# Performance work log

Measured on AMD Instinct MI355X. Metric: run time of the kernel, lower is better.

The kernel has to match this reference:

```python
import jax, jax.numpy as jnp
import numpy as np

CLASS_W, COORD_W = 2.0, 5.0
ALPHA, GAMMA = 0.25, 2.0
NUM_SAMPLE_POINTS = 100
MATCH_NUM = 13
INF = 1e8


def _bernstein_matrix(n):
    t = jnp.linspace(0.0, 1.0, n, dtype=jnp.float32)
    return jnp.stack([(1 - t) ** 3, 3 * t * (1 - t) ** 2,
                      3 * t ** 2 * (1 - t), t ** 3], axis=1)  # [n, 4]


def _sample_bezier(ctrl):  # ctrl: [N, 4, 2] -> [N, n*2]
    B = _bernstein_matrix(NUM_SAMPLE_POINTS)
    pts = jnp.einsum('sk,nkd->nsd', B, ctrl)
    return pts.reshape(ctrl.shape[0], -1)


def setup_inputs() -> dict:
    key = jax.random.key(0)
    k1, k2, k3, k4 = jax.random.split(key, 4)
    bs, nq, nc, n_gt = 4, 1000, 1, 32
    return {
        'pred_logits': jax.random.normal(k1, (bs, nq, nc), dtype=jnp.float32),
        'pred_beziers': jax.random.uniform(k2, (bs, nq, 8), dtype=jnp.float32),
        'tgt_labels': jax.random.randint(k3, (bs, n_gt), 0, nc).astype(jnp.int64),
        'tgt_beziers': jax.random.uniform(k4, (bs, n_gt, 4, 2), dtype=jnp.float32),
    }


def _cost_matrix(pred_logits, pred_beziers, tgt_labels, tgt_beziers):
    bs, nq, nc = pred_logits.shape
    n_gt = tgt_labels.shape[1]
    out_prob = jax.nn.sigmoid(pred_logits.reshape(bs * nq, nc))
    tgt_ids = tgt_labels.reshape(-1)
    neg = (1 - ALPHA) * out_prob ** GAMMA * (-jnp.log1p(-out_prob + 1e-8))
    pos = ALPHA * (1 - out_prob) ** GAMMA * (-jnp.log(out_prob + 1e-8))
    cost_class = pos[:, tgt_ids] - neg[:, tgt_ids]        # [bs*nq, bs*n_gt]
    out_pts = _sample_bezier(pred_beziers.reshape(-1, 4, 2))   # [bs*nq, S*2]
    tgt_pts = _sample_bezier(tgt_beziers.reshape(-1, 4, 2))    # [bs*n_gt, S*2]
    cost_coord = jnp.sum(jnp.abs(out_pts[:, None, :] - tgt_pts[None, :, :]), axis=-1)
    C = CLASS_W * cost_class + COORD_W * cost_coord       # [bs*nq, bs*n_gt]
    C4 = C.reshape(bs, nq, bs, n_gt)
    # per-image block (equivalent of C.split(sizes, -1) with c[i])
    return C4[jnp.arange(bs), :, jnp.arange(bs), :]       # [bs, nq, n_gt]


def _assign(c):  # c: [nq, n_gt]
    nq, n_gt = c.shape
    # k smallest queries per target (torch.topk largest=False along dim 0)
    _, idx = jax.lax.top_k(-c.T, MATCH_NUM)               # [n_gt, k]
    src = idx.reshape(-1)                                  # [n_gt*k]
    cols = jnp.repeat(jnp.arange(n_gt), MATCH_NUM)
    cost_inf = jnp.full((nq, n_gt), INF, dtype=c.dtype)
    cost_inf = cost_inf.at[src, cols].set(c[src, cols])
    min_idx = jnp.argmin(cost_inf, axis=1)                 # [nq]
    # sorted unique of src, padded with sentinel nq (jit-friendly torch.unique)
    s = jnp.sort(src)
    keep = jnp.concatenate([jnp.array([True]), s[1:] != s[:-1]])
    uniq = jnp.sort(jnp.where(keep, s, nq))
    count = keep.sum().astype(jnp.int32)
    tgt = jnp.where(uniq < nq, min_idx[jnp.clip(uniq, 0, nq - 1)], -1)
    return uniq, tgt, count


def reference(pred_logits, pred_beziers, tgt_labels, tgt_beziers):
    c = _cost_matrix(pred_logits, pred_beziers, tgt_labels, tgt_beziers)
    src_u, tgt_u, counts = jax.vmap(_assign)(c)
    # src_u/tgt_u: [bs, n_gt*MATCH_NUM], valid entries = first counts[i], rest padded
    return src_u, tgt_u, counts
```

## Files before the change

kernel.cpp:

```cpp
#include <hip/hip_runtime.h>
#include <stdint.h>

#define NQ 1000
#define NGT 32
#define BS 4
#define NSP 100
#define MNUM 13
#define NPAIR (NGT * MNUM)
#define QPB 8

__device__ __forceinline__ unsigned int f2sort(float f) {
    unsigned int u = __float_as_uint(f);
    return (u & 0x80000000u) ? ~u : (u | 0x80000000u);
}

__global__ __launch_bounds__(256) void cost_kernel(
    const float* __restrict__ logits,
    const float* __restrict__ pbez,
    const float* __restrict__ tbez,
    float* __restrict__ C)
{
    const int blk = blockIdx.x;
    const int b  = blk / (NQ / QPB);
    const int qc = blk % (NQ / QPB);
    const int tid = threadIdx.x;

    __shared__ float tpts[NGT][201];
    __shared__ float ppts[QPB][201];
    __shared__ float cls[QPB];

    for (int idx = tid; idx < NGT * NSP; idx += 256) {
        const int g = idx / NSP, s = idx % NSP;
        const float t   = (float)s * (1.0f / 99.0f);
        const float omt = 1.0f - t;
        const float b0 = omt * omt * omt;
        const float b1 = 3.0f * t * omt * omt;
        const float b2 = 3.0f * t * t * omt;
        const float b3 = t * t * t;
        const float* c8 = tbez + ((size_t)b * NGT + g) * 8;
        tpts[g][2 * s]     = b0 * c8[0] + b1 * c8[2] + b2 * c8[4] + b3 * c8[6];
        tpts[g][2 * s + 1] = b0 * c8[1] + b1 * c8[3] + b2 * c8[5] + b3 * c8[7];
    }
    for (int idx = tid; idx < QPB * NSP; idx += 256) {
        const int ql = idx / NSP, s = idx % NSP;
        const int q = qc * QPB + ql;
        const float t   = (float)s * (1.0f / 99.0f);
        const float omt = 1.0f - t;
        const float b0 = omt * omt * omt;
        const float b1 = 3.0f * t * omt * omt;
        const float b2 = 3.0f * t * t * omt;
        const float b3 = t * t * t;
        const float* c8 = pbez + ((size_t)b * NQ + q) * 8;
        ppts[ql][2 * s]     = b0 * c8[0] + b1 * c8[2] + b2 * c8[4] + b3 * c8[6];
        ppts[ql][2 * s + 1] = b0 * c8[1] + b1 * c8[3] + b2 * c8[5] + b3 * c8[7];
    }
    if (tid < QPB) {
        const int q = qc * QPB + tid;
        const float lg = logits[(size_t)b * NQ + q];
        float p;
        if (lg >= 0.0f) { p = 1.0f / (1.0f + expf(-lg)); }
        else            { const float e = expf(lg); p = e / (1.0f + e); }
        const float pos = 0.25f * (1.0f - p) * (1.0f - p) * (-logf(p + 1e-8f));
        const float neg = 0.75f * p * p * (-log1pf(-p + 1e-8f));
        cls[tid] = pos - neg;
    }
    __syncthreads();

    const int ql = tid >> 5;
    const int g  = tid & 31;
    double acc = 0.0;
    #pragma unroll 8
    for (int i = 0; i < 2 * NSP; ++i)
        acc += (double)fabsf(ppts[ql][i] - tpts[g][i]);
    const int q = qc * QPB + ql;
    C[((size_t)b * NQ + q) * NGT + g] = 2.0f * cls[ql] + 5.0f * (float)acc;
}

__global__ __launch_bounds__(64) void select_kernel(
    const float* __restrict__ C,
    int* __restrict__ sel)
{
    const int blk = blockIdx.x;
    const int b = blk / NGT, g = blk % NGT;
    const int lane = threadIdx.x;

    unsigned long long loc[16];
    #pragma unroll
    for (int j = 0; j < 16; ++j) {
        const int q = j * 64 + lane;
        if (q < NQ) {
            const float c = C[((size_t)b * NQ + q) * NGT + g];
            loc[j] = ((unsigned long long)f2sort(c) << 32) | (unsigned int)q;
        } else {
            loc[j] = ~0ull;
        }
    }
    for (int r = 0; r < MNUM; ++r) {
        unsigned long long m = loc[0];
        #pragma unroll
        for (int j = 1; j < 16; ++j) m = (loc[j] < m) ? loc[j] : m;
        #pragma unroll
        for (int off = 1; off < 64; off <<= 1) {
            const unsigned long long o = __shfl_xor(m, off, 64);
            m = (o < m) ? o : m;
        }
        const int q = (int)(m & 0xFFFFFFFFu);
        if (lane == (q & 63)) loc[q >> 6] = ~0ull;
        if (lane == 0) sel[blk * MNUM + r] = q;
    }
}

__global__ __launch_bounds__(256) void assemble_kernel(
    const float* __restrict__ C,
    const int* __restrict__ sel,
    int* __restrict__ out)
{
    const int b = blockIdx.x;
    const int tid = threadIdx.x;

    __shared__ unsigned long long key[NQ];
    __shared__ int cnts[256];
    __shared__ int offs[257];

    for (int q = tid; q < NQ; q += 256) key[q] = ~0ull;
    __syncthreads();

    for (int j = tid; j < NPAIR; j += 256) {
        const int g = j / MNUM;
        const int q = sel[(b * NGT + g) * MNUM + (j % MNUM)];
        const float c = C[((size_t)b * NQ + q) * NGT + g];
        const unsigned long long k =
            ((unsigned long long)f2sort(c) << 32) | (unsigned int)g;
        atomicMin(&key[q], k);
    }
    __syncthreads();

    const int base = tid * 4;
    int lc = 0;
    for (int k = 0; k < 4; ++k) {
        const int q = base + k;
        if (q < NQ && key[q] != ~0ull) lc++;
    }
    cnts[tid] = lc;
    __syncthreads();
    if (tid == 0) {
        int run = 0;
        for (int i = 0; i < 256; ++i) { offs[i] = run; run += cnts[i]; }
        offs[256] = run;
    }
    __syncthreads();

    const int total = offs[256];
    int* src_out = out + b * NPAIR;
    int* tgt_out = out + BS * NPAIR + b * NPAIR;

    int pos = offs[tid];
    for (int k = 0; k < 4; ++k) {
        const int q = base + k;
        if (q < NQ && key[q] != ~0ull) {
            src_out[pos] = q;
            tgt_out[pos] = (int)(key[q] & 0xFFFFFFFFu);
            pos++;
        }
    }
    for (int i = total + tid; i < NPAIR; i += 256) {
        src_out[i] = NQ;
        tgt_out[i] = -1;
    }
    if (tid == 0) out[2 * BS * NPAIR + b] = total;
}

extern "C" void kernel_launch(void* const* d_in, const int* in_sizes, int n_in,
                              void* d_out, int out_size, void* d_ws, size_t ws_size,
                              hipStream_t stream) {
    const float* logits = (const float*)d_in[0];
    const float* pbez   = (const float*)d_in[1];
    const float* tbez   = (const float*)d_in[3];

    float* C   = (float*)d_ws;
    int*   sel = (int*)((char*)d_ws + (size_t)BS * NQ * NGT * sizeof(float));
    int*   out = (int*)d_out;

    cost_kernel<<<BS * (NQ / QPB), 256, 0, stream>>>(logits, pbez, tbez, C);
    select_kernel<<<BS * NGT, 64, 0, stream>>>(C, sel);
    assemble_kernel<<<BS, 256, 0, stream>>>(C, sel, out);
}
```

Baseline: 86.33 us.

## Fuse cost, top-k select and assemble into one kernel with per-image flag sync

Replaces the three-kernel pipeline with one kernel in which each block owns one (image, target) column. The block computes that column of the cost matrix in shared memory, recomputing each query's Bezier samples on the fly, then runs the 13-smallest selection locally. The selected indices and sort keys go to a workspace, and one block per image spins on MAGIC flags before doing the unique/argmin assembly. This removes two launches and the global cost-matrix round trip. In exchange, each prediction curve is sampled 32 times instead of once. Correctness relies on all blocks being co-resident for the spin-wait, and the flags are never reset, so a later call can see stale MAGIC values.

```diff
diff --git a/kernel.cpp b/kernel.cpp
--- a/kernel.cpp
+++ b/kernel.cpp
@@ -7,131 +7,139 @@
 #define NSP 100
 #define MNUM 13
 #define NPAIR (NGT * MNUM)
-#define QPB 8
+#define MAGIC 0x5A5A5A5Au
+
+#define SEL_WORDS 32
+#define FLAG_BASE (128 * SEL_WORDS)
 
 __device__ __forceinline__ unsigned int f2sort(float f) {
     unsigned int u = __float_as_uint(f);
     return (u & 0x80000000u) ? ~u : (u | 0x80000000u);
 }
 
-__global__ __launch_bounds__(256) void cost_kernel(
+__global__ __launch_bounds__(256) void fused_matcher_kernel(
     const float* __restrict__ logits,
     const float* __restrict__ pbez,
     const float* __restrict__ tbez,
-    float* __restrict__ C)
+    unsigned int* __restrict__ ws,
+    int* __restrict__ out)
 {
     const int blk = blockIdx.x;
-    const int b  = blk / (NQ / QPB);
-    const int qc = blk % (NQ / QPB);
+    const int b = blk >> 5;
+    const int g = blk & 31;
     const int tid = threadIdx.x;
 
-    __shared__ float tpts[NGT][201];
-    __shared__ float ppts[QPB][201];
-    __shared__ float cls[QPB];
+    __shared__ float bas[NSP][4];
+    __shared__ float tp[2 * NSP];
+    __shared__ float colC[NQ];
+    __shared__ int          selq_s[MNUM];
+    __shared__ unsigned int selk_s[MNUM];
+    __shared__ unsigned long long key[NQ];
+    __shared__ int cnts[256];
+    __shared__ int offs[257];
 
-    for (int idx = tid; idx < NGT * NSP; idx += 256) {
-        const int g = idx / NSP, s = idx % NSP;
-        const float t   = (float)s * (1.0f / 99.0f);
+    if (tid < NSP) {
+        const float t   = (float)tid * (1.0f / 99.0f);
         const float omt = 1.0f - t;
         const float b0 = omt * omt * omt;
         const float b1 = 3.0f * t * omt * omt;
         const float b2 = 3.0f * t * t * omt;
         const float b3 = t * t * t;
+        bas[tid][0] = b0; bas[tid][1] = b1; bas[tid][2] = b2; bas[tid][3] = b3;
         const float* c8 = tbez + ((size_t)b * NGT + g) * 8;
-        tpts[g][2 * s]     = b0 * c8[0] + b1 * c8[2] + b2 * c8[4] + b3 * c8[6];
-        tpts[g][2 * s + 1] = b0 * c8[1] + b1 * c8[3] + b2 * c8[5] + b3 * c8[7];
-    }
-    for (int idx = tid; idx < QPB * NSP; idx += 256) {
-        const int ql = idx / NSP, s = idx % NSP;
-        const int q = qc * QPB + ql;
-        const float t   = (float)s * (1.0f / 99.0f);
-        const float omt = 1.0f - t;
-        const float b0 = omt * omt * omt;
-        const float b1 = 3.0f * t * omt * omt;
-        const float b2 = 3.0f * t * t * omt;
-        const float b3 = t * t * t;
-        const float* c8 = pbez + ((size_t)b * NQ + q) * 8;
-        ppts[ql][2 * s]     = b0 * c8[0] + b1 * c8[2] + b2 * c8[4] + b3 * c8[6];
-        ppts[ql][2 * s + 1] = b0 * c8[1] + b1 * c8[3] + b2 * c8[5] + b3 * c8[7];
-    }
-    if (tid < QPB) {
-        const int q = qc * QPB + tid;
-        const float lg = logits[(size_t)b * NQ + q];
-        float p;
-        if (lg >= 0.0f) { p = 1.0f / (1.0f + expf(-lg)); }
-        else            { const float e = expf(lg); p = e / (1.0f + e); }
-        const float pos = 0.25f * (1.0f - p) * (1.0f - p) * (-logf(p + 1e-8f));
-        const float neg = 0.75f * p * p * (-log1pf(-p + 1e-8f));
-        cls[tid] = pos - neg;
+        tp[2 * tid]     = b0 * c8[0] + b1 * c8[2] + b2 * c8[4] + b3 * c8[6];
+        tp[2 * tid + 1] = b0 * c8[1] + b1 * c8[3] + b2 * c8[5] + b3 * c8[7];
     }
     __syncthreads();
 
-    const int ql = tid >> 5;
-    const int g  = tid & 31;
-    double acc = 0.0;
-    #pragma unroll 8
-    for (int i = 0; i < 2 * NSP; ++i)
-        acc += (double)fabsf(ppts[ql][i] - tpts[g][i]);
-    const int q = qc * QPB + ql;
-    C[((size_t)b * NQ + q) * NGT + g] = 2.0f * cls[ql] + 5.0f * (float)acc;
-}
-
-__global__ __launch_bounds__(64) void select_kernel(
-    const float* __restrict__ C,
-    int* __restrict__ sel)
-{
-    const int blk = blockIdx.x;
-    const int b = blk / NGT, g = blk % NGT;
-    const int lane = threadIdx.x;
-
-    unsigned long long loc[16];
-    #pragma unroll
-    for (int j = 0; j < 16; ++j) {
-        const int q = j * 64 + lane;
-        if (q < NQ) {
-            const float c = C[((size_t)b * NQ + q) * NGT + g];
-            loc[j] = ((unsigned long long)f2sort(c) << 32) | (unsigned int)q;
-        } else {
-            loc[j] = ~0ull;
+    if (tid < 250) {
+        float ctrl[4][8];
+        const float4* pb = (const float4*)(pbez + ((size_t)b * NQ + tid * 4) * 8);
+        #pragma unroll
+        for (int k = 0; k < 4; ++k) {
+            const float4 u = pb[2 * k], v = pb[2 * k + 1];
+            ctrl[k][0] = u.x; ctrl[k][1] = u.y; ctrl[k][2] = u.z; ctrl[k][3] = u.w;
+            ctrl[k][4] = v.x; ctrl[k][5] = v.y; ctrl[k][6] = v.z; ctrl[k][7] = v.w;
+        }
+        double acc[4] = {0.0, 0.0, 0.0, 0.0};
+        for (int s = 0; s < NSP; ++s) {
+            const float b0 = bas[s][0], b1 = bas[s][1], b2 = bas[s][2], b3 = bas[s][3];
+            const float tx = tp[2 * s], ty = tp[2 * s + 1];
+            #pragma unroll
+            for (int k = 0; k < 4; ++k) {
+                const float px = b0 * ctrl[k][0] + b1 * ctrl[k][2] + b2 * ctrl[k][4] + b3 * ctrl[k][6];
+                const float py = b0 * ctrl[k][1] + b1 * ctrl[k][3] + b2 * ctrl[k][5] + b3 * ctrl[k][7];
+                acc[k] += (double)fabsf(px - tx);
+                acc[k] += (double)fabsf(py - ty);
+            }
+        }
+        const float4 lg4 = *(const float4*)(logits + (size_t)b * NQ + tid * 4);
+        const float lgs[4] = {lg4.x, lg4.y, lg4.z, lg4.w};
+        #pragma unroll
+        for (int k = 0; k < 4; ++k) {
+            const float lg = lgs[k];
+            float p;
+            if (lg >= 0.0f) { p = 1.0f / (1.0f + expf(-lg)); }
+            else            { const float e = expf(lg); p = e / (1.0f + e); }
+            const float pos = 0.25f * (1.0f - p) * (1.0f - p) * (-logf(p + 1e-8f));
+            const float neg = 0.75f * p * p * (-log1pf(-p + 1e-8f));
+            colC[tid * 4 + k] = 2.0f * (pos - neg) + 5.0f * (float)acc[k];
         }
     }
-    for (int r = 0; r < MNUM; ++r) {
-        unsigned long long m = loc[0];
+    __syncthreads();
+
+    if (tid < 64) {
+        unsigned long long loc[16];
         #pragma unroll
-        for (int j = 1; j < 16; ++j) m = (loc[j] < m) ? loc[j] : m;
-        #pragma unroll
-        for (int off = 1; off < 64; off <<= 1) {
-            const unsigned long long o = __shfl_xor(m, off, 64);
-            m = (o < m) ? o : m;
+        for (int j = 0; j < 16; ++j) {
+            const int q = j * 64 + tid;
+            loc[j] = (q < NQ)
+                ? (((unsigned long long)f2sort(colC[q]) << 32) | (unsigned int)q)
+                : ~0ull;
         }
-        const int q = (int)(m & 0xFFFFFFFFu);
-        if (lane == (q & 63)) loc[q >> 6] = ~0ull;
-        if (lane == 0) sel[blk * MNUM + r] = q;
+        for (int r = 0; r < MNUM; ++r) {
+            unsigned long long m = loc[0];
+            #pragma unroll
+            for (int j = 1; j < 16; ++j) m = (loc[j] < m) ? loc[j] : m;
+            #pragma unroll
+            for (int off = 1; off < 64; off <<= 1) {
+                const unsigned long long o = __shfl_xor(m, off, 64);
+                m = (o < m) ? o : m;
+            }
+            const int q = (int)(m & 0xFFFFFFFFu);
+            if (tid == (q & 63)) loc[q >> 6] = ~0ull;
+            if (tid == 0) { selq_s[r] = q; selk_s[r] = (unsigned int)(m >> 32); }
+        }
     }
-}
+    __syncthreads();
 
-__global__ __launch_bounds__(256) void assemble_kernel(
-    const float* __restrict__ C,
-    const int* __restrict__ sel,
-    int* __restrict__ out)
-{
-    const int b = blockIdx.x;
-    const int tid = threadIdx.x;
+    unsigned int* selws = ws + blk * SEL_WORDS;
+    if (tid < MNUM)                      selws[tid]      = (unsigned int)selq_s[tid];
+    if (tid >= 16 && tid < 16 + MNUM)    selws[tid]      = selk_s[tid - 16];
+    __threadfence();
+    __syncthreads();
+    if (tid == 0) atomicExch(ws + FLAG_BASE + blk, MAGIC);
 
-    __shared__ unsigned long long key[NQ];
-    __shared__ int cnts[256];
-    __shared__ int offs[257];
+    if (g != 0) return;
+
+    if (tid >= 1 && tid < NGT) {
+        while (__hip_atomic_load(ws + FLAG_BASE + b * NGT + tid,
+                                 __ATOMIC_RELAXED, __HIP_MEMORY_SCOPE_AGENT) != MAGIC) {
+            __builtin_amdgcn_s_sleep(1);
+        }
+    }
+    __syncthreads();
+    __threadfence();
 
     for (int q = tid; q < NQ; q += 256) key[q] = ~0ull;
     __syncthreads();
 
     for (int j = tid; j < NPAIR; j += 256) {
-        const int g = j / MNUM;
-        const int q = sel[(b * NGT + g) * MNUM + (j % MNUM)];
-        const float c = C[((size_t)b * NQ + q) * NGT + g];
-        const unsigned long long k =
-            ((unsigned long long)f2sort(c) << 32) | (unsigned int)g;
-        atomicMin(&key[q], k);
+        const int gg = j / MNUM, r = j % MNUM;
+        const unsigned int* sw = ws + (b * NGT + gg) * SEL_WORDS;
+        const unsigned int q   = sw[r];
+        const unsigned int k32 = sw[16 + r];
+        atomicMin(&key[q], ((unsigned long long)k32 << 32) | (unsigned int)gg);
     }
     __syncthreads();
 
@@ -177,11 +185,6 @@
     const float* pbez   = (const float*)d_in[1];
     const float* tbez   = (const float*)d_in[3];
 
-    float* C   = (float*)d_ws;
-    int*   sel = (int*)((char*)d_ws + (size_t)BS * NQ * NGT * sizeof(float));
-    int*   out = (int*)d_out;
-
-    cost_kernel<<<BS * (NQ / QPB), 256, 0, stream>>>(logits, pbez, tbez, C);
-    select_kernel<<<BS * NGT, 64, 0, stream>>>(C, sel);
-    assemble_kernel<<<BS, 256, 0, stream>>>(C, sel, out);
+    fused_matcher_kernel<<<BS * NGT, 256, 0, stream>>>(
+        logits, pbez, tbez, (unsigned int*)d_ws, (int*)d_out);
 }
```

New measurement: 89.89 us. 4.1% more time.

## Fuse top-k selection and assembly into one per-image kernel with wave scan

Applied to the files above, without the earlier changes.

Merges the per-target selection kernel and the assembly kernel into a single 1024-thread block per image. Each wave handles two targets in sequence, and the selected indices and keys go to shared memory, so the global sel buffer round trip and the re-read of C are gone. The serial 256-entry prefix sum is replaced by a wave-level shuffle scan over 16 partial sums. The trade-off is that selection now runs on only 4 blocks instead of 128, which cuts parallelism, and each wave does two targets serially.

```diff
diff --git a/kernel.cpp b/kernel.cpp
--- a/kernel.cpp
+++ b/kernel.cpp
@@ -76,94 +76,84 @@
     C[((size_t)b * NQ + q) * NGT + g] = 2.0f * cls[ql] + 5.0f * (float)acc;
 }
 
-__global__ __launch_bounds__(64) void select_kernel(
+__global__ __launch_bounds__(1024) void select_assemble_kernel(
     const float* __restrict__ C,
-    int* __restrict__ sel)
-{
-    const int blk = blockIdx.x;
-    const int b = blk / NGT, g = blk % NGT;
-    const int lane = threadIdx.x;
-
-    unsigned long long loc[16];
-    #pragma unroll
-    for (int j = 0; j < 16; ++j) {
-        const int q = j * 64 + lane;
-        if (q < NQ) {
-            const float c = C[((size_t)b * NQ + q) * NGT + g];
-            loc[j] = ((unsigned long long)f2sort(c) << 32) | (unsigned int)q;
-        } else {
-            loc[j] = ~0ull;
-        }
-    }
-    for (int r = 0; r < MNUM; ++r) {
-        unsigned long long m = loc[0];
-        #pragma unroll
-        for (int j = 1; j < 16; ++j) m = (loc[j] < m) ? loc[j] : m;
-        #pragma unroll
-        for (int off = 1; off < 64; off <<= 1) {
-            const unsigned long long o = __shfl_xor(m, off, 64);
-            m = (o < m) ? o : m;
-        }
-        const int q = (int)(m & 0xFFFFFFFFu);
-        if (lane == (q & 63)) loc[q >> 6] = ~0ull;
-        if (lane == 0) sel[blk * MNUM + r] = q;
-    }
-}
-
-__global__ __launch_bounds__(256) void assemble_kernel(
-    const float* __restrict__ C,
-    const int* __restrict__ sel,
     int* __restrict__ out)
 {
-    const int b = blockIdx.x;
+    const int b   = blockIdx.x;
     const int tid = threadIdx.x;
+    const int wid  = tid >> 6;
+    const int lane = tid & 63;
 
+    __shared__ int          selq[NGT][MNUM];
+    __shared__ unsigned int selk[NGT][MNUM];
     __shared__ unsigned long long key[NQ];
-    __shared__ int cnts[256];
-    __shared__ int offs[257];
+    __shared__ int wsum[16];
+    __shared__ int total_s;
 
-    for (int q = tid; q < NQ; q += 256) key[q] = ~0ull;
-    __syncthreads();
+    for (int q = tid; q < NQ; q += 1024) key[q] = ~0ull;
 
-    for (int j = tid; j < NPAIR; j += 256) {
-        const int g = j / MNUM;
-        const int q = sel[(b * NGT + g) * MNUM + (j % MNUM)];
-        const float c = C[((size_t)b * NQ + q) * NGT + g];
-        const unsigned long long k =
-            ((unsigned long long)f2sort(c) << 32) | (unsigned int)g;
-        atomicMin(&key[q], k);
+    for (int half = 0; half < 2; ++half) {
+        const int g = wid + 16 * half;
+        unsigned long long loc[16];
+        #pragma unroll
+        for (int j = 0; j < 16; ++j) {
+            const int q = j * 64 + lane;
+            loc[j] = (q < NQ)
+                ? (((unsigned long long)f2sort(C[((size_t)b * NQ + q) * NGT + g]) << 32)
+                   | (unsigned int)q)
+                : ~0ull;
+        }
+        for (int r = 0; r < MNUM; ++r) {
+            unsigned long long m = loc[0];
+            #pragma unroll
+            for (int j = 1; j < 16; ++j) m = (loc[j] < m) ? loc[j] : m;
+            #pragma unroll
+            for (int off = 1; off < 64; off <<= 1) {
+                const unsigned long long o = __shfl_xor(m, off, 64);
+                m = (o < m) ? o : m;
+            }
+            const int q = (int)(m & 0xFFFFFFFFu);
+            if (lane == (q & 63)) loc[q >> 6] = ~0ull;
+            if (lane == 0) { selq[g][r] = q; selk[g][r] = (unsigned int)(m >> 32); }
+        }
     }
     __syncthreads();
 
-    const int base = tid * 4;
-    int lc = 0;
-    for (int k = 0; k < 4; ++k) {
-        const int q = base + k;
-        if (q < NQ && key[q] != ~0ull) lc++;
+    if (tid < NPAIR) {
+        const int g = tid / MNUM, r = tid % MNUM;
+        atomicMin(&key[selq[g][r]],
+                  ((unsigned long long)selk[g][r] << 32) | (unsigned int)g);
     }
-    cnts[tid] = lc;
+    __syncthreads();
+
+    const int flag = (tid < NQ && key[tid] != ~0ull) ? 1 : 0;
+    int scan = flag;
+    #pragma unroll
+    for (int d = 1; d < 64; d <<= 1) {
+        const int o = __shfl_up(scan, d, 64);
+        if (lane >= d) scan += o;
+    }
+    if (lane == 63) wsum[wid] = scan;
     __syncthreads();
     if (tid == 0) {
         int run = 0;
-        for (int i = 0; i < 256; ++i) { offs[i] = run; run += cnts[i]; }
-        offs[256] = run;
+        #pragma unroll
+        for (int i = 0; i < 16; ++i) { const int v = wsum[i]; wsum[i] = run; run += v; }
+        total_s = run;
     }
     __syncthreads();
 
-    const int total = offs[256];
+    const int total = total_s;
     int* src_out = out + b * NPAIR;
     int* tgt_out = out + BS * NPAIR + b * NPAIR;
 
-    int pos = offs[tid];
-    for (int k = 0; k < 4; ++k) {
-        const int q = base + k;
-        if (q < NQ && key[q] != ~0ull) {
-            src_out[pos] = q;
-            tgt_out[pos] = (int)(key[q] & 0xFFFFFFFFu);
-            pos++;
-        }
+    if (flag) {
+        const int pos = wsum[wid] + scan - 1;
+        src_out[pos] = tid;
+        tgt_out[pos] = (int)(key[tid] & 0xFFFFFFFFu);
     }
-    for (int i = total + tid; i < NPAIR; i += 256) {
+    for (int i = total + tid; i < NPAIR; i += 1024) {
         src_out[i] = NQ;
         tgt_out[i] = -1;
     }
@@ -177,11 +167,7 @@
     const float* pbez   = (const float*)d_in[1];
     const float* tbez   = (const float*)d_in[3];
 
-    float* C   = (float*)d_ws;
-    int*   sel = (int*)((char*)d_ws + (size_t)BS * NQ * NGT * sizeof(float));
-    int*   out = (int*)d_out;
-
+    float* C = (float*)d_ws;
     cost_kernel<<<BS * (NQ / QPB), 256, 0, stream>>>(logits, pbez, tbez, C);
-    select_kernel<<<BS * NGT, 64, 0, stream>>>(C, sel);
-    assemble_kernel<<<BS, 256, 0, stream>>>(C, sel, out);
+    select_assemble_kernel<<<BS, 1024, 0, stream>>>(C, (int*)d_out);
 }
```

Result: slower. 101.3 us (+17.4%).
